# Kernel optimization log

Hardware: AMD Instinct MI355X
Metric: run time of the kernel (lower is better)

## Reference

```python
import jax, jax.numpy as jnp
import numpy as np

DIM = 512
HEADS = 8
HEAD_DIM = DIM // HEADS  # 64
NUM_ENC = 32             # num_encoding_channels
ENC_RANGE = 1.0
OFFSETS = (0, 512, 2560) # B=2 point clouds, num_points=(512, 2048)
B = len(OFFSETS) - 1
M = 2048                 # max num_points -> padded length
TOTAL = OFFSETS[-1]      # 2560 total points
ENC_IN = NUM_ENC * 3 + 3 # 99 (concat_input=True)


def setup_inputs() -> dict:
    key = jax.random.key(0)
    ks = jax.random.split(key, 6)
    return {
        "features": jax.random.normal(ks[0], (TOTAL, DIM), jnp.float32),
        "coordinates": jax.random.uniform(ks[1], (TOTAL, 3), jnp.float32),
        "qkv_w": jax.random.normal(ks[2], (3 * DIM, DIM), jnp.float32) * (DIM ** -0.5),
        "proj_w": jax.random.normal(ks[3], (DIM, DIM), jnp.float32) * (DIM ** -0.5),
        "proj_b": jnp.zeros((DIM,), jnp.float32),
        "pos_w": jax.random.normal(ks[4], (HEAD_DIM, ENC_IN), jnp.float32) * (ENC_IN ** -0.5),
        "pos_b": jnp.zeros((HEAD_DIM,), jnp.float32),
        "offsets": jnp.array(OFFSETS, jnp.int32),
    }


def reference(features, coordinates, qkv_w, proj_w, proj_b, pos_w, pos_b, offsets):
    # ragged -> padded index math (replaces cat_to_pad / pad_to_cat Python loops)
    pt = jnp.arange(TOTAL)
    b_idx = jnp.searchsorted(offsets, pt, side='right') - 1   # batch id per point
    w_idx = pt - offsets[b_idx]                                # within-batch position
    num_points = offsets[1:] - offsets[:-1]                    # [B]

    # SinusoidalEncoding(num_channels=32, concat_input=True) + Linear -> head_dim
    half = NUM_ENC // 2
    freqs = (2.0 ** jnp.arange(half, dtype=jnp.float32)) * jnp.pi / ENC_RANGE
    sc = coordinates[..., None] * freqs                        # [T, 3, half]
    enc = jnp.concatenate([jnp.sin(sc), jnp.cos(sc)], -1).reshape(TOTAL, 3 * NUM_ENC)
    enc = jnp.concatenate([enc, coordinates], -1)              # [T, 99]
    pos = enc @ pos_w.T + pos_b                                # [T, head_dim]

    feat_pad = jnp.zeros((B, M, DIM), features.dtype).at[b_idx, w_idx].set(features)
    pos_pad = jnp.zeros((B, M, HEAD_DIM), pos.dtype).at[b_idx, w_idx].set(pos)

    # offset_to_mask: mask[b, :, :offsets[b], :offsets[b]] = -inf (cumulative offsets!)
    r = jnp.arange(M)
    off_b = offsets[:-1]                                       # [B]
    blocked = (r[None, :, None] < off_b[:, None, None]) & (r[None, None, :] < off_b[:, None, None])
    mask = jnp.where(blocked, -jnp.inf, 0.0)[:, None]          # [B, 1, M, M]

    # attention
    qkv = (feat_pad @ qkv_w.T).reshape(B, M, 3, HEADS, HEAD_DIM)
    qkv = jnp.transpose(qkv, (2, 0, 3, 1, 4))                  # [3, B, H, M, hd]
    q, k, v = qkv[0], qkv[1], qkv[2]
    q = q + pos_pad[:, None]                                   # broadcast over heads
    k = k + pos_pad[:, None]
    scale = HEAD_DIM ** -0.5
    scores = jnp.einsum('bhqd,bhkd->bhqk', q, k) * scale + mask
    attn = jax.nn.softmax(scores, axis=-1)
    y = jnp.einsum('bhqk,bhkd->bhqd', attn, v)                 # [B, H, M, hd]
    y = jnp.transpose(y, (0, 2, 1, 3)).reshape(B, M, DIM)
    y = y @ proj_w.T + proj_b

    # zero_out_points: x[b, num_points[b]:] = 0
    valid = r[None, :] < num_points[:, None]
    y = jnp.where(valid[..., None], y, 0.0)

    # pad_to_cat back to ragged [total_N, C]
    return y[b_idx, w_idx]
```

## Files before the change

kernel.cpp:

```cpp
#include <hip/hip_runtime.h>
#include <math.h>

#define TOTAL 2560
#define NEG_BIG (-1e30f)
#define LOG2E_8 0.18033688011112042f

typedef __bf16 bf16x8 __attribute__((ext_vector_type(8)));
typedef float f32x4 __attribute__((ext_vector_type(4)));
typedef unsigned short ushort8v __attribute__((ext_vector_type(8)));
typedef unsigned short ushort4v __attribute__((ext_vector_type(4)));

__device__ inline unsigned short f2bf(float f) {
    unsigned u = __builtin_bit_cast(unsigned, f);
    u += 0x7fff + ((u >> 16) & 1);
    return (unsigned short)(u >> 16);
}

__device__ inline void gload16(const void* g, void* l) {
    __builtin_amdgcn_global_load_lds(
        (const __attribute__((address_space(1))) void*)g,
        (__attribute__((address_space(3))) void*)l, 16, 0, 0);
}

__global__ __launch_bounds__(256) void pos_cast_kernel(
    const float* __restrict__ coords,
    const float* __restrict__ pos_w,
    const float* __restrict__ pos_b,
    const float* __restrict__ f,  const float* __restrict__ qw, const float* __restrict__ pw,
    float* __restrict__ pos_out,
    unsigned short* __restrict__ fb, unsigned short* __restrict__ qwb, unsigned short* __restrict__ pwb)
{
    const int bx = blockIdx.x;
    if (bx < 640) {
        __shared__ float enc[4][100];
        const int wv   = threadIdx.x >> 6;
        const int lane = threadIdx.x & 63;
        const int p = bx * 4 + wv;
        const float c0 = coords[p * 3 + 0];
        const float c1 = coords[p * 3 + 1];
        const float c2 = coords[p * 3 + 2];
        for (int i = lane; i < 99; i += 64) {
            float v;
            if (i < 96) {
                const int d = i >> 5;
                const int j = i & 31;
                const float cv = (d == 0) ? c0 : ((d == 1) ? c1 : c2);
                const float freq = exp2f((float)(j & 15)) * 3.14159265358979323846f;
                const float sc = cv * freq;
                v = (j < 16) ? sinf(sc) : cosf(sc);
            } else {
                v = (i == 96) ? c0 : ((i == 97) ? c1 : c2);
            }
            enc[wv][i] = v;
        }
        float acc = pos_b[lane];
        const float* w = pos_w + lane * 99;
        for (int i = 0; i < 99; ++i) acc = fmaf(enc[wv][i], w[i], acc);
        pos_out[p * 64 + lane] = acc;
    } else {
        const int s = (bx - 640) * 256 + threadIdx.x;
        const float* src; unsigned short* dst; int ls;
        if (s < 163840)      { src = f;  dst = fb;  ls = s; }
        else if (s < 262144) { src = qw; dst = qwb; ls = s - 163840; }
        else                 { src = pw; dst = pwb; ls = s - 262144; }
        const float4 x0 = *(const float4*)(src + ls * 8);
        const float4 x1 = *(const float4*)(src + ls * 8 + 4);
        ushort8v o;
        o[0] = f2bf(x0.x); o[1] = f2bf(x0.y); o[2] = f2bf(x0.z); o[3] = f2bf(x0.w);
        o[4] = f2bf(x1.x); o[5] = f2bf(x1.y); o[6] = f2bf(x1.z); o[7] = f2bf(x1.w);
        *(ushort8v*)(dst + ls * 8) = o;
    }
}

__global__ __launch_bounds__(256) void qkv_mfma_kernel(
    const unsigned short* __restrict__ A,
    const unsigned short* __restrict__ Bm,
    const float* __restrict__ pos,
    unsigned short* __restrict__ q_ws,
    unsigned short* __restrict__ k_ws,
    unsigned short* __restrict__ vt_ws)
{
    __shared__ unsigned short Abuf[2][64 * 64];
    __shared__ unsigned short Bbuf[2][64 * 64];
    const int m0 = blockIdx.x * 64;
    const int n0 = blockIdx.y * 64;
    const int t = threadIdx.x;
    const int w = t >> 6, lane = t & 63;
    const int wr = w >> 1, wc = w & 1;
    const int c = lane & 15, g = lane >> 4;

    auto STAGE = [&](int kt, int cur) {
#pragma unroll
        for (int i = 0; i < 2; ++i) {
            const int off = w * 2048 + i * 1024;
            const int ba  = off + lane * 16;
            const int row = ba >> 7;
            const int slot = (ba & 127) >> 4;
            gload16(A  + (m0 + row) * 512 + kt * 64 + ((slot ^ (row & 7)) * 8),
                    (char*)&Abuf[cur][0] + off);
            gload16(Bm + (n0 + row) * 512 + kt * 64 + ((slot ^ (row & 7)) * 8),
                    (char*)&Bbuf[cur][0] + off);
        }
    };

    f32x4 acc[2][2];
#pragma unroll
    for (int mi = 0; mi < 2; ++mi)
#pragma unroll
        for (int ni = 0; ni < 2; ++ni) acc[mi][ni] = (f32x4){0.f, 0.f, 0.f, 0.f};

    STAGE(0, 0);
    int cur = 0;
    for (int kt = 0; kt < 8; ++kt) {
        __syncthreads();
        if (kt + 1 < 8) STAGE(kt + 1, cur ^ 1);
#pragma unroll
        for (int kk = 0; kk < 2; ++kk) {
            bf16x8 af[2], bfr[2];
#pragma unroll
            for (int mi = 0; mi < 2; ++mi) {
                const int row = wr * 32 + mi * 16 + c;
                af[mi] = *(const bf16x8*)&Abuf[cur][row * 64 + ((g + 4 * kk) ^ (row & 7)) * 8];
            }
#pragma unroll
            for (int ni = 0; ni < 2; ++ni) {
                const int row = wc * 32 + ni * 16 + c;
                bfr[ni] = *(const bf16x8*)&Bbuf[cur][row * 64 + ((g + 4 * kk) ^ (row & 7)) * 8];
            }
#pragma unroll
            for (int mi = 0; mi < 2; ++mi)
#pragma unroll
                for (int ni = 0; ni < 2; ++ni)
                    acc[mi][ni] = __builtin_amdgcn_mfma_f32_16x16x32_bf16(af[mi], bfr[ni], acc[mi][ni], 0, 0, 0);
        }
        cur ^= 1;
    }

    const int which = n0 >> 9;
    const int h = (n0 >> 6) & 7;
#pragma unroll
    for (int mi = 0; mi < 2; ++mi)
#pragma unroll
        for (int ni = 0; ni < 2; ++ni) {
            const int dd = wc * 32 + ni * 16 + c;
            const int p0 = m0 + wr * 32 + mi * 16 + 4 * g;
            if (which == 2) {
                ushort4v o4;
#pragma unroll
                for (int r = 0; r < 4; ++r) o4[r] = f2bf(acc[mi][ni][r]);
                *(ushort4v*)(vt_ws + (h * 64 + dd) * TOTAL + p0) = o4;
            } else {
#pragma unroll
                for (int r = 0; r < 4; ++r) {
                    const int p = p0 + r;
                    const float v = acc[mi][ni][r] + pos[p * 64 + dd];
                    const int idx = (h * TOTAL + p) * 64 + dd;
                    if (which == 0) q_ws[idx] = f2bf(v);
                    else            k_ws[idx] = f2bf(v);
                }
            }
        }
}

__global__ __launch_bounds__(512) void attn_kernel(
    const unsigned short* __restrict__ q_ws,
    const unsigned short* __restrict__ k_ws,
    const unsigned short* __restrict__ vt_ws,
    unsigned short* __restrict__ y)
{
    const int bx = blockIdx.x;
    const int h  = bx & 7;
    const int qt = bx >> 3;

    const int t    = threadIdx.x;
    const int w    = t >> 6;
    const int wp   = w & 3;
    const int half = w >> 2;
    const int koff = half * 128;
    const int lane = t & 63;
    const int g    = lane >> 4;
    const int c    = lane & 15;
    const int c7   = c & 7;

    __shared__ unsigned short Kbuf[256 * 64];
    __shared__ unsigned short Vbuf[2][64 * 256];
    __shared__ unsigned short P_lds[64][264];
    __shared__ float  Om[64 * 64];
    __shared__ float2 Oml[64];

    const int nphase = (qt < 8) ? 2 : 1;
    int cur = 0;

    for (int phase = 0; phase < nphase; ++phase) {
        const int base = phase ? 0 : 512;
        const int nkt  = phase ? 2 : 8;
        const int kt0  = (!phase && qt < 8) ? 2 : 0;
        const float extra = phase ? 1536.0f : 0.0f;

        const unsigned short* Kg = k_ws + (h * TOTAL + base) * 64;
        const unsigned short* Vg = vt_ws + h * 64 * TOTAL + base;

        const unsigned short* Qrow = q_ws + ((h * TOTAL) + base + qt * 64 + 16 * wp + c) * 64;
        const bf16x8 qa0 = *(const bf16x8*)(Qrow + 8 * g);
        const bf16x8 qa1 = *(const bf16x8*)(Qrow + 8 * g + 32);

        float m_old = NEG_BIG, l_old = 0.f;
        f32x4 o_acc[4];
#pragma unroll
        for (int n = 0; n < 4; ++n) o_acc[n] = (f32x4){0.f, 0.f, 0.f, 0.f};

        auto STAGE_K = [&](int kt) {
#pragma unroll
            for (int i = 0; i < 4; ++i) {
                const int off = w * 4096 + i * 1024;
                const int ba  = off + lane * 16;
                const int row = ba >> 7;
                const int slot = (ba & 127) >> 4;
                gload16(Kg + (kt * 256 + row) * 64 + ((slot ^ (row & 7)) * 8),
                        (char*)&Kbuf[0] + off);
            }
        };
        auto STAGE_V = [&](int kt, int vb) {
#pragma unroll
            for (int i = 0; i < 4; ++i) {
                const int off = w * 4096 + i * 1024;
                const int ba  = off + lane * 16;
                const int dd  = ba >> 9;
                const int slot = (ba & 511) >> 4;
                gload16(Vg + dd * TOTAL + kt * 256 + ((slot ^ (dd & 7)) * 8),
                        (char*)&Vbuf[vb][0] + off);
            }
        };

        if (phase) __syncthreads();
        STAGE_K(kt0);
        STAGE_V(kt0, cur);

        for (int kt = kt0; kt < nkt; ++kt) {
            __syncthreads();

            f32x4 s_acc[8];
#pragma unroll
            for (int n = 0; n < 8; ++n) {
                const int row = koff + 16 * n + c;
                const bf16x8 kb0 = *(const bf16x8*)&Kbuf[row * 64 + ((g + 0) ^ c7) * 8];
                const bf16x8 kb1 = *(const bf16x8*)&Kbuf[row * 64 + ((g + 4) ^ c7) * 8];
                f32x4 a = __builtin_amdgcn_mfma_f32_16x16x32_bf16(kb0, qa0, (f32x4){0.f,0.f,0.f,0.f}, 0, 0, 0);
                s_acc[n] = __builtin_amdgcn_mfma_f32_16x16x32_bf16(kb1, qa1, a, 0, 0, 0);
            }
            __syncthreads();
            if (kt + 1 < nkt) STAGE_K(kt + 1);

            f32x4 m4 = s_acc[0];
#pragma unroll
            for (int n = 1; n < 8; ++n)
#pragma unroll
                for (int r = 0; r < 4; ++r) m4[r] = fmaxf(m4[r], s_acc[n][r]);
            float tm = fmaxf(fmaxf(m4[0], m4[1]), fmaxf(m4[2], m4[3])) * LOG2E_8;
            tm = fmaxf(tm, __shfl_xor(tm, 16));
            tm = fmaxf(tm, __shfl_xor(tm, 32));
            if (!__all(tm <= m_old + 8.0f)) {
                const float m_new = fmaxf(m_old, tm);
                const float corr = exp2f(m_old - m_new);
                float corr_r[4];
#pragma unroll
                for (int r = 0; r < 4; ++r) corr_r[r] = __shfl(corr, 4 * g + r);
#pragma unroll
                for (int n = 0; n < 4; ++n)
#pragma unroll
                    for (int r = 0; r < 4; ++r) o_acc[n][r] *= corr_r[r];
                l_old *= corr;
                m_old = m_new;
            }
            float rs = 0.f;
#pragma unroll
            for (int n = 0; n < 8; ++n)
#pragma unroll
                for (int r = 0; r < 4; ++r) {
                    const float pv = exp2f(fmaf(s_acc[n][r], LOG2E_8, -m_old));
                    s_acc[n][r] = pv;
                    rs += pv;
                }
            rs += __shfl_xor(rs, 16);
            rs += __shfl_xor(rs, 32);
            l_old += rs;

#pragma unroll
            for (int n = 0; n < 8; ++n) {
                ushort4v pk;
#pragma unroll
                for (int r = 0; r < 4; ++r) pk[r] = f2bf(s_acc[n][r]);
                *(ushort4v*)&P_lds[16 * wp + c][koff + 16 * n + 4 * g] = pk;
            }

            if (kt + 1 < nkt) STAGE_V(kt + 1, cur ^ 1);

#pragma unroll
            for (int kk = 0; kk < 4; ++kk) {
                const bf16x8 pa = *(const bf16x8*)&P_lds[16 * wp + c][koff + 8 * g + 32 * kk];
                const int vgrp = ((koff >> 3) + 4 * kk + g) ^ c7;
#pragma unroll
                for (int n = 0; n < 4; ++n) {
                    const bf16x8 vb = *(const bf16x8*)&Vbuf[cur][(16 * n + c) * 256 + vgrp * 8];
                    o_acc[n] = __builtin_amdgcn_mfma_f32_16x16x32_bf16(pa, vb, o_acc[n], 0, 0, 0);
                }
            }
            cur ^= 1;
        }

        if (half == 1) {
            const int pr = wp * 16;
#pragma unroll
            for (int n = 0; n < 4; ++n)
#pragma unroll
                for (int r = 0; r < 4; ++r)
                    Om[(pr + 4 * g + r) * 64 + 16 * n + c] = o_acc[n][r];
            if (g == 0) Oml[pr + c] = make_float2(m_old, l_old);
        }
        __syncthreads();
        if (half == 0) {
            const int pr = wp * 16;
            const float2 o2 = Oml[pr + c];
            const float mm = fmaxf(m_old, o2.x);
            const float f0 = exp2f(m_old - mm), f1 = exp2f(o2.x - mm);
            float l = l_old * f0 + o2.y * f1;
            float so = 1.f;
            if (extra > 0.f) {
                const float mn = fmaxf(mm, 0.f);
                const float cc = exp2f(mm - mn);
                l = l * cc + extra * exp2f(-mn);
                so = cc;
            }
            const float inv = so / l;
            const float a0 = f0 * inv, a1 = f1 * inv;
            float a0r[4], a1r[4];
#pragma unroll
            for (int r = 0; r < 4; ++r) {
                a0r[r] = __shfl(a0, 4 * g + r);
                a1r[r] = __shfl(a1, 4 * g + r);
            }
            unsigned short* yb = y + (base + qt * 64 + 16 * wp) * 512 + h * 64;
#pragma unroll
            for (int n = 0; n < 4; ++n)
#pragma unroll
                for (int r = 0; r < 4; ++r) {
                    const float o1v = Om[(pr + 4 * g + r) * 64 + 16 * n + c];
                    yb[(4 * g + r) * 512 + 16 * n + c] =
                        f2bf(o_acc[n][r] * a0r[r] + o1v * a1r[r]);
                }
        }
    }
}

__global__ __launch_bounds__(256) void proj_mfma_kernel(
    const unsigned short* __restrict__ A,
    const unsigned short* __restrict__ Bm,
    const float* __restrict__ bias,
    float* __restrict__ out)
{
    __shared__ unsigned short Abuf[2][64 * 64];
    __shared__ unsigned short Bbuf[2][64 * 64];
    const int m0 = blockIdx.x * 64;
    const int n0 = blockIdx.y * 64;
    const int t = threadIdx.x;
    const int w = t >> 6, lane = t & 63;
    const int wr = w >> 1, wc = w & 1;
    const int c = lane & 15, g = lane >> 4;

    auto STAGE = [&](int kt, int cur) {
#pragma unroll
        for (int i = 0; i < 2; ++i) {
            const int off = w * 2048 + i * 1024;
            const int ba  = off + lane * 16;
            const int row = ba >> 7;
            const int slot = (ba & 127) >> 4;
            gload16(A  + (m0 + row) * 512 + kt * 64 + ((slot ^ (row & 7)) * 8),
                    (char*)&Abuf[cur][0] + off);
            gload16(Bm + (n0 + row) * 512 + kt * 64 + ((slot ^ (row & 7)) * 8),
                    (char*)&Bbuf[cur][0] + off);
        }
    };

    f32x4 acc[2][2];
#pragma unroll
    for (int mi = 0; mi < 2; ++mi)
#pragma unroll
        for (int ni = 0; ni < 2; ++ni) acc[mi][ni] = (f32x4){0.f, 0.f, 0.f, 0.f};

    STAGE(0, 0);
    int cur = 0;
    for (int kt = 0; kt < 8; ++kt) {
        __syncthreads();
        if (kt + 1 < 8) STAGE(kt + 1, cur ^ 1);
#pragma unroll
        for (int kk = 0; kk < 2; ++kk) {
            bf16x8 af[2], bfr[2];
#pragma unroll
            for (int mi = 0; mi < 2; ++mi) {
                const int row = wr * 32 + mi * 16 + c;
                af[mi] = *(const bf16x8*)&Abuf[cur][row * 64 + ((g + 4 * kk) ^ (row & 7)) * 8];
            }
#pragma unroll
            for (int ni = 0; ni < 2; ++ni) {
                const int row = wc * 32 + ni * 16 + c;
                bfr[ni] = *(const bf16x8*)&Bbuf[cur][row * 64 + ((g + 4 * kk) ^ (row & 7)) * 8];
            }
#pragma unroll
            for (int mi = 0; mi < 2; ++mi)
#pragma unroll
                for (int ni = 0; ni < 2; ++ni)
                    acc[mi][ni] = __builtin_amdgcn_mfma_f32_16x16x32_bf16(af[mi], bfr[ni], acc[mi][ni], 0, 0, 0);
        }
        cur ^= 1;
    }

#pragma unroll
    for (int mi = 0; mi < 2; ++mi)
#pragma unroll
        for (int ni = 0; ni < 2; ++ni) {
            const int col = n0 + wc * 32 + ni * 16 + c;
            const float bv = bias[col];
#pragma unroll
            for (int r = 0; r < 4; ++r) {
                const int p = m0 + wr * 32 + mi * 16 + 4 * g + r;
                out[p * 512 + col] = acc[mi][ni][r] + bv;
            }
        }
}

extern "C" void kernel_launch(void* const* d_in, const int* in_sizes, int n_in,
                              void* d_out, int out_size, void* d_ws, size_t ws_size,
                              hipStream_t stream) {
    const float* features = (const float*)d_in[0];
    const float* coords   = (const float*)d_in[1];
    const float* qkv_w    = (const float*)d_in[2];
    const float* proj_w   = (const float*)d_in[3];
    const float* proj_b   = (const float*)d_in[4];
    const float* pos_w    = (const float*)d_in[5];
    const float* pos_b    = (const float*)d_in[6];
    float* out = (float*)d_out;

    float* pos_ws = (float*)d_ws;
    unsigned short* feat_bf  = (unsigned short*)(pos_ws + TOTAL * 64);
    unsigned short* qkvw_bf  = feat_bf + 2560 * 512;
    unsigned short* projw_bf = qkvw_bf + 1536 * 512;
    unsigned short* q_ws  = projw_bf + 512 * 512;
    unsigned short* k_ws  = q_ws  + 8 * TOTAL * 64;
    unsigned short* vt_ws = k_ws  + 8 * TOTAL * 64;
    unsigned short* y_bf  = vt_ws + 8 * TOTAL * 64;

    pos_cast_kernel<<<dim3(1792), dim3(256), 0, stream>>>(
        coords, pos_w, pos_b, features, qkv_w, proj_w,
        pos_ws, feat_bf, qkvw_bf, projw_bf);
    qkv_mfma_kernel<<<dim3(40, 24), dim3(256), 0, stream>>>(
        feat_bf, qkvw_bf, pos_ws, q_ws, k_ws, vt_ws);
    attn_kernel<<<dim3(256), dim3(512), 0, stream>>>(q_ws, k_ws, vt_ws, y_bf);
    proj_mfma_kernel<<<dim3(40, 8), dim3(256), 0, stream>>>(
        y_bf, projw_bf, proj_b, out);
}
```

Baseline: 58.03 us.

## Split attention key tile across four wave groups with 1024-thread blocks

```diff
diff --git a/kernel.cpp b/kernel.cpp
--- a/kernel.cpp
+++ b/kernel.cpp
@@ -162,7 +162,7 @@
         }
 }
 
-__global__ __launch_bounds__(512) void attn_kernel(
+__global__ __launch_bounds__(1024) void attn_kernel(
     const unsigned short* __restrict__ q_ws,
     const unsigned short* __restrict__ k_ws,
     const unsigned short* __restrict__ vt_ws,
@@ -175,8 +175,8 @@
     const int t    = threadIdx.x;
     const int w    = t >> 6;
     const int wp   = w & 3;
-    const int half = w >> 2;
-    const int koff = half * 128;
+    const int qu   = w >> 2;
+    const int koff = qu * 64;
     const int lane = t & 63;
     const int g    = lane >> 4;
     const int c    = lane & 15;
@@ -185,8 +185,7 @@
     __shared__ unsigned short Kbuf[256 * 64];
     __shared__ unsigned short Vbuf[2][64 * 256];
     __shared__ unsigned short P_lds[64][264];
-    __shared__ float  Om[64 * 64];
-    __shared__ float2 Oml[64];
+    __shared__ float2 Oml[3][64];
 
     const int nphase = (qt < 8) ? 2 : 1;
     int cur = 0;
@@ -211,8 +210,8 @@
 
         auto STAGE_K = [&](int kt) {
 #pragma unroll
-            for (int i = 0; i < 4; ++i) {
-                const int off = w * 4096 + i * 1024;
+            for (int i = 0; i < 2; ++i) {
+                const int off = w * 2048 + i * 1024;
                 const int ba  = off + lane * 16;
                 const int row = ba >> 7;
                 const int slot = (ba & 127) >> 4;
@@ -222,8 +221,8 @@
         };
         auto STAGE_V = [&](int kt, int vb) {
 #pragma unroll
-            for (int i = 0; i < 4; ++i) {
-                const int off = w * 4096 + i * 1024;
+            for (int i = 0; i < 2; ++i) {
+                const int off = w * 2048 + i * 1024;
                 const int ba  = off + lane * 16;
                 const int dd  = ba >> 9;
                 const int slot = (ba & 511) >> 4;
@@ -239,9 +238,9 @@
         for (int kt = kt0; kt < nkt; ++kt) {
             __syncthreads();
 
-            f32x4 s_acc[8];
-#pragma unroll
-            for (int n = 0; n < 8; ++n) {
+            f32x4 s_acc[4];
+#pragma unroll
+            for (int n = 0; n < 4; ++n) {
                 const int row = koff + 16 * n + c;
                 const bf16x8 kb0 = *(const bf16x8*)&Kbuf[row * 64 + ((g + 0) ^ c7) * 8];
                 const bf16x8 kb1 = *(const bf16x8*)&Kbuf[row * 64 + ((g + 4) ^ c7) * 8];
@@ -253,7 +252,7 @@
 
             f32x4 m4 = s_acc[0];
 #pragma unroll
-            for (int n = 1; n < 8; ++n)
+            for (int n = 1; n < 4; ++n)
 #pragma unroll
                 for (int r = 0; r < 4; ++r) m4[r] = fmaxf(m4[r], s_acc[n][r]);
             float tm = fmaxf(fmaxf(m4[0], m4[1]), fmaxf(m4[2], m4[3])) * LOG2E_8;
@@ -274,7 +273,7 @@
             }
             float rs = 0.f;
 #pragma unroll
-            for (int n = 0; n < 8; ++n)
+            for (int n = 0; n < 4; ++n)
 #pragma unroll
                 for (int r = 0; r < 4; ++r) {
                     const float pv = exp2f(fmaf(s_acc[n][r], LOG2E_8, -m_old));
@@ -286,7 +285,7 @@
             l_old += rs;
 
 #pragma unroll
-            for (int n = 0; n < 8; ++n) {
+            for (int n = 0; n < 4; ++n) {
                 ushort4v pk;
 #pragma unroll
                 for (int r = 0; r < 4; ++r) pk[r] = f2bf(s_acc[n][r]);
@@ -296,9 +295,9 @@
             if (kt + 1 < nkt) STAGE_V(kt + 1, cur ^ 1);
 
 #pragma unroll
-            for (int kk = 0; kk < 4; ++kk) {
+            for (int kk = 0; kk < 2; ++kk) {
                 const bf16x8 pa = *(const bf16x8*)&P_lds[16 * wp + c][koff + 8 * g + 32 * kk];
-                const int vgrp = ((koff >> 3) + 4 * kk + g) ^ c7;
+                const int vgrp = (qu * 8 + 4 * kk + g) ^ c7;
 #pragma unroll
                 for (int n = 0; n < 4; ++n) {
                     const bf16x8 vb = *(const bf16x8*)&Vbuf[cur][(16 * n + c) * 256 + vgrp * 8];
@@ -308,22 +307,27 @@
             cur ^= 1;
         }
 
-        if (half == 1) {
-            const int pr = wp * 16;
+        __syncthreads();
+        float* scr = (float*)&Vbuf[0][0];
+        if (qu != 0) {
+            float* s0 = scr + (qu - 1) * 4096;
 #pragma unroll
             for (int n = 0; n < 4; ++n)
 #pragma unroll
                 for (int r = 0; r < 4; ++r)
-                    Om[(pr + 4 * g + r) * 64 + 16 * n + c] = o_acc[n][r];
-            if (g == 0) Oml[pr + c] = make_float2(m_old, l_old);
+                    s0[(16 * wp + 4 * g + r) * 64 + 16 * n + c] = o_acc[n][r];
+            if (g == 0) Oml[qu - 1][16 * wp + c] = make_float2(m_old, l_old);
         }
         __syncthreads();
-        if (half == 0) {
-            const int pr = wp * 16;
-            const float2 o2 = Oml[pr + c];
-            const float mm = fmaxf(m_old, o2.x);
-            const float f0 = exp2f(m_old - mm), f1 = exp2f(o2.x - mm);
-            float l = l_old * f0 + o2.y * f1;
+        if (qu == 0) {
+            const int row = 16 * wp + c;
+            const float2 q1 = Oml[0][row];
+            const float2 q2 = Oml[1][row];
+            const float2 q3 = Oml[2][row];
+            const float mm = fmaxf(fmaxf(m_old, q1.x), fmaxf(q2.x, q3.x));
+            const float f0 = exp2f(m_old - mm), f1 = exp2f(q1.x - mm);
+            const float f2 = exp2f(q2.x - mm), f3 = exp2f(q3.x - mm);
+            float l = l_old * f0 + q1.y * f1 + q2.y * f2 + q3.y * f3;
             float so = 1.f;
             if (extra > 0.f) {
                 const float mn = fmaxf(mm, 0.f);
@@ -332,21 +336,26 @@
                 so = cc;
             }
             const float inv = so / l;
-            const float a0 = f0 * inv, a1 = f1 * inv;
-            float a0r[4], a1r[4];
+            const float a0 = f0 * inv, a1 = f1 * inv, a2 = f2 * inv, a3 = f3 * inv;
+            float a0r[4], a1r[4], a2r[4], a3r[4];
 #pragma unroll
             for (int r = 0; r < 4; ++r) {
                 a0r[r] = __shfl(a0, 4 * g + r);
                 a1r[r] = __shfl(a1, 4 * g + r);
+                a2r[r] = __shfl(a2, 4 * g + r);
+                a3r[r] = __shfl(a3, 4 * g + r);
             }
             unsigned short* yb = y + (base + qt * 64 + 16 * wp) * 512 + h * 64;
 #pragma unroll
             for (int n = 0; n < 4; ++n)
 #pragma unroll
                 for (int r = 0; r < 4; ++r) {
-                    const float o1v = Om[(pr + 4 * g + r) * 64 + 16 * n + c];
-                    yb[(4 * g + r) * 512 + 16 * n + c] =
-                        f2bf(o_acc[n][r] * a0r[r] + o1v * a1r[r]);
+                    const int ro = (16 * wp + 4 * g + r) * 64 + 16 * n + c;
+                    float o = o_acc[n][r] * a0r[r];
+                    o += scr[ro] * a1r[r];
+                    o += scr[4096 + ro] * a2r[r];
+                    o += scr[8192 + ro] * a3r[r];
+                    yb[(4 * g + r) * 512 + 16 * n + c] = f2bf(o);
                 }
         }
     }
@@ -454,7 +463,7 @@
         pos_ws, feat_bf, qkvw_bf, projw_bf);
     qkv_mfma_kernel<<<dim3(40, 24), dim3(256), 0, stream>>>(
         feat_bf, qkvw_bf, pos_ws, q_ws, k_ws, vt_ws);
-    attn_kernel<<<dim3(256), dim3(512), 0, stream>>>(q_ws, k_ws, vt_ws, y_bf);
+    attn_kernel<<<dim3(256), dim3(1024), 0, stream>>>(q_ws, k_ws, vt_ws, y_bf);
     proj_mfma_kernel<<<dim3(40, 8), dim3(256), 0, stream>>>(
         y_bf, projw_bf, proj_b, out);
 }
```

After: 57.95 us. No clear change (-0.1%).
